# Kernel tuning notes

Measured on AMD Instinct MI355X. Metric: run time of the kernel, lower is better.

The kernel has to match this reference:

```python
import jax, jax.numpy as jnp
import numpy as np

DIM = 768
H = 12
HEAD = DIM // H
SCALE = HEAD ** -0.5
NMM, NV, NA = 8, 4, 4


def _cross_attn(x1, x2, qw, kvw, pw, pb):
    # x1: [B,N1,C] queries, x2: [B,N2,C] keys/values. Weights stored [in,out].
    B, N1, C = x1.shape
    N2 = x2.shape[1]
    q = (x1 @ qw).reshape(B, N1, H, HEAD).transpose(0, 2, 1, 3)        # [B,H,N1,d]
    kv = (x2 @ kvw).reshape(B, N2, 2, H, HEAD)
    k = kv[:, :, 0].transpose(0, 2, 1, 3)                               # [B,H,N2,d]
    v = kv[:, :, 1].transpose(0, 2, 1, 3)
    attn = jax.nn.softmax(jnp.einsum('bhnd,bhmd->bhnm', q, k) * SCALE, axis=-1)
    o = jnp.einsum('bhnm,bhmd->bhnd', attn, v).transpose(0, 2, 1, 3).reshape(B, N1, C)
    return o @ pw + pb, attn


def setup_inputs() -> dict:
    key = jax.random.key(0)
    ks = jax.random.split(key, 16)
    s = 0.02
    inp = {
        'xmm': jax.random.normal(ks[0], (64, 16, DIM), jnp.float32),
        'xv': jax.random.normal(ks[1], (64, 784, DIM), jnp.float32),
        'xa': jax.random.normal(ks[2], (64, 512, DIM), jnp.float32),
        # visual cross-attn params (weights stored [in,out] = torch W.T)
        'qv_w': s * jax.random.normal(ks[3], (DIM, DIM), jnp.float32),
        'kvv_w': s * jax.random.normal(ks[4], (DIM, 2 * DIM), jnp.float32),
        'projv_w': s * jax.random.normal(ks[5], (DIM, DIM), jnp.float32),
        'projv_b': jnp.zeros((DIM,), jnp.float32),
        # audio cross-attn params
        'qa_w': s * jax.random.normal(ks[6], (DIM, DIM), jnp.float32),
        'kva_w': s * jax.random.normal(ks[7], (DIM, 2 * DIM), jnp.float32),
        'proja_w': s * jax.random.normal(ks[8], (DIM, DIM), jnp.float32),
        'proja_b': jnp.zeros((DIM,), jnp.float32),
        # factorized fusion attention params (dim_ratio=1.0 -> inner dim = DIM)
        'fq_w': s * jax.random.normal(ks[9], (DIM, DIM), jnp.float32),
        'fk_w': s * jax.random.normal(ks[10], (2 * DIM, DIM), jnp.float32),
        'fv_w': s * jax.random.normal(ks[11], (2 * DIM, DIM), jnp.float32),
        'fproj_w': s * jax.random.normal(ks[12], (DIM, DIM), jnp.float32),
        'fproj_b': jnp.zeros((DIM,), jnp.float32),
    }
    return inp


def reference(xmm, xv, xa, qv_w, kvv_w, projv_w, projv_b,
              qa_w, kva_w, proja_w, proja_b,
              fq_w, fk_w, fv_w, fproj_w, fproj_b):
    B = xmm.shape[0]
    xmm2 = xmm[:, :NMM]
    xmm_v, _ = _cross_attn(xmm[:, NMM:NMM + NV], xv, qv_w, kvv_w, projv_w, projv_b)
    xmm_a, _ = _cross_attn(xmm[:, NMM + NV:], xa, qa_w, kva_w, proja_w, proja_b)
    # outer-product token fusion: [B, NV*NA, 2*DIM]
    xva = jnp.concatenate([
        jnp.broadcast_to(xmm_v[:, :, None, :], (B, NV, NA, DIM)),
        jnp.broadcast_to(xmm_a[:, None, :, :], (B, NV, NA, DIM)),
    ], axis=-1).reshape(B, NV * NA, 2 * DIM)
    q = (xmm2 @ fq_w).reshape(B, NMM, H, -1).transpose(0, 2, 1, 3)
    k = (xva @ fk_w).reshape(B, NV * NA, H, -1).transpose(0, 2, 1, 3)
    v = (xva @ fv_w).reshape(B, NV * NA, H, -1).transpose(0, 2, 1, 3)
    attn = jax.nn.softmax(jnp.einsum('bhnd,bhmd->bhnm', q, k) * SCALE, axis=-1)
    o = jnp.einsum('bhnm,bhmd->bhnd', attn, v).transpose(0, 2, 1, 3).reshape(B, NMM, DIM)
    o = o @ fproj_w + fproj_b
    xmm_out = jnp.concatenate([o, xmm_v, xmm_a], axis=1)  # [B,16,DIM]
    return xmm_out, attn
```

## Files before the change

kernel.cpp:

```cpp
#include <hip/hip_runtime.h>
#include <stdint.h>

typedef unsigned short u16;
typedef unsigned int u32;
typedef __attribute__((ext_vector_type(8))) short short8;
typedef __attribute__((ext_vector_type(4))) float floatx4;


__device__ __forceinline__ u16 f2bf_rne(float f) {
  u32 u = __float_as_uint(f);
  return (u16)((u + 0x7fffu + ((u >> 16) & 1u)) >> 16);
}
__device__ __forceinline__ u32 pack_rne_u(u32 a, u32 b) {
  a += 0x7fffu + ((a >> 16) & 1u);
  b += 0x7fffu + ((b >> 16) & 1u);
  return __builtin_amdgcn_perm(b, a, 0x07060302u);
}
__device__ __forceinline__ void gld_lds16(const void* g, void* l) {
  __builtin_amdgcn_global_load_lds(
      (__attribute__((address_space(1))) void*)(uintptr_t)g,
      (__attribute__((address_space(3))) void*)l, 16, 0, 0);
}

__device__ __forceinline__ void sg_body(
    float (*sAt)[20], float (*sW)[64],
    const float* __restrict__ A, int a_pitch, int a_rb, int a_off,
    const float* __restrict__ W, const float* __restrict__ bias,
    float* __restrict__ Cout, int c_pitch, int c_rb, int c_off,
    int rt, int n0)
{
  const int t = threadIdx.x;
  const int g = t >> 6;
  const int c = t & 63;

  float acc[4] = {0.f, 0.f, 0.f, 0.f};

  for (int ks = 0; ks < 12; ++ks) {
    {
      int r = t >> 4;
      int c4 = (t & 15) * 4;
      int lr = rt * 16 + r;
      int grow = (lr / a_rb) * a_pitch + a_off + (lr % a_rb);
      float4 v = *(const float4*)(A + (size_t)grow * 768 + ks * 64 + c4);
      sAt[c4 + 0][r] = v.x;
      sAt[c4 + 1][r] = v.y;
      sAt[c4 + 2][r] = v.z;
      sAt[c4 + 3][r] = v.w;
    }
#pragma unroll
    for (int u = 0; u < 4; ++u) {
      int unit = t + u * 256;
      int r = unit >> 4;
      int c4 = (unit & 15) * 4;
      *(float4*)&sW[r][c4] = *(const float4*)(W + (size_t)(ks * 64 + r) * 768 + n0 + c4);
    }
    __syncthreads();
#pragma unroll 8
    for (int k = 0; k < 64; ++k) {
      float4 a4 = *(const float4*)&sAt[k][g * 4];
      float w = sW[k][c];
      acc[0] += a4.x * w;
      acc[1] += a4.y * w;
      acc[2] += a4.z * w;
      acc[3] += a4.w * w;
    }
    __syncthreads();
  }

  float bs = bias ? bias[n0 + c] : 0.f;
#pragma unroll
  for (int rr = 0; rr < 4; ++rr) {
    int lr = rt * 16 + g * 4 + rr;
    int grow = (lr / c_rb) * c_pitch + c_off + (lr % c_rb);
    Cout[(size_t)grow * 768 + n0 + c] = acc[rr] + bs;
  }
}

__global__ __launch_bounds__(256) void qproj(
    const float* __restrict__ xmm,
    const float* __restrict__ qv_w, const float* __restrict__ qa_w,
    const float* __restrict__ fq_w,
    float* __restrict__ q_v, float* __restrict__ q_a, float* __restrict__ q_f)
{
  __shared__ float sAt[64][20];
  __shared__ float sW[64][64];
  int rt = blockIdx.x;
  int n0 = blockIdx.y * 64;
  if (rt < 16)
    sg_body(sAt, sW, xmm, 16, 4, 8, qv_w, nullptr, q_v, 4, 4, 0, rt, n0);
  else if (rt < 32)
    sg_body(sAt, sW, xmm, 16, 4, 12, qa_w, nullptr, q_a, 4, 4, 0, rt - 16, n0);
  else
    sg_body(sAt, sW, xmm, 16, 8, 0, fq_w, nullptr, q_f, 8, 8, 0, rt - 32, n0);
}

__global__ __launch_bounds__(256) void proj2(
    const float* __restrict__ o_v, const float* __restrict__ o_a,
    const float* __restrict__ projv_w, const float* __restrict__ projv_b,
    const float* __restrict__ proja_w, const float* __restrict__ proja_b,
    float* __restrict__ out0)
{
  __shared__ float sAt[64][20];
  __shared__ float sW[64][64];
  int z = blockIdx.z;
  sg_body(sAt, sW, z ? o_a : o_v, 4, 4, 0,
          z ? proja_w : projv_w, z ? proja_b : projv_b,
          out0, 16, 4, z ? 12 : 8, blockIdx.x, blockIdx.y * 64);
}

__global__ __launch_bounds__(256) void fkv(
    const float* __restrict__ out0,
    const float* __restrict__ fk_w, const float* __restrict__ fv_w,
    float* __restrict__ kbase)
{
  __shared__ float sAt[64][20];
  __shared__ float sW[64][64];
  int z = blockIdx.z;
  const float* W = (z < 2) ? (fk_w + (size_t)(z & 1) * 768 * 768)
                           : (fv_w + (size_t)(z & 1) * 768 * 768);
  int a_off = (z & 1) ? 12 : 8;
  sg_body(sAt, sW, out0, 16, 4, a_off, W, nullptr,
          kbase + (size_t)z * 256 * 768, 4, 4, 0, blockIdx.x, blockIdx.y * 64);
}

__global__ __launch_bounds__(256) void fproj(
    const float* __restrict__ o_f,
    const float* __restrict__ fproj_w, const float* __restrict__ fproj_b,
    float* __restrict__ out0)
{
  __shared__ float sAt[64][20];
  __shared__ float sW[64][64];
  sg_body(sAt, sW, o_f, 8, 8, 0, fproj_w, fproj_b, out0, 16, 8, 0,
          blockIdx.x, blockIdx.y * 64);
}

__global__ __launch_bounds__(256) void qtilde(
    const float* __restrict__ q_v, const float* __restrict__ q_a,
    const float* __restrict__ kvv_w, const float* __restrict__ kva_w,
    u16* __restrict__ Qt_v, u16* __restrict__ Qt_a)
{
  __shared__ float sAt[64][20];
  __shared__ float sW[64][65];

  const int rt = blockIdx.x;
  const int nt = blockIdx.y;
  const int path = blockIdx.z / 12;
  const int h = blockIdx.z % 12;
  const float* q = path ? q_a : q_v;
  const float* kvw = path ? kva_w : kvv_w;
  u16* Qt = path ? Qt_a : Qt_v;

  const int t = threadIdx.x;
  const int g = t >> 6;
  const int c = t & 63;
  const int n0 = nt * 64;

  {
    int r = t >> 4;
    int c4 = (t & 15) * 4;
    float4 v = *(const float4*)(q + (size_t)(rt * 16 + r) * 768 + h * 64 + c4);
    sAt[c4 + 0][r] = v.x;
    sAt[c4 + 1][r] = v.y;
    sAt[c4 + 2][r] = v.z;
    sAt[c4 + 3][r] = v.w;
  }
#pragma unroll
  for (int u = 0; u < 4; ++u) {
    int unit = t + u * 256;
    int d = unit >> 4;
    int c4 = (unit & 15) * 4;
    float4 v = *(const float4*)(kvw + (size_t)(n0 + d) * 1536 + h * 64 + c4);
    sW[d][c4 + 0] = v.x;
    sW[d][c4 + 1] = v.y;
    sW[d][c4 + 2] = v.z;
    sW[d][c4 + 3] = v.w;
  }
  __syncthreads();

  float acc[4] = {0.f, 0.f, 0.f, 0.f};
#pragma unroll 16
  for (int e = 0; e < 64; ++e) {
    float4 a4 = *(const float4*)&sAt[e][g * 4];
    float w = sW[c][e];
    acc[0] += a4.x * w;
    acc[1] += a4.y * w;
    acc[2] += a4.z * w;
    acc[3] += a4.w * w;
  }
#pragma unroll
  for (int rr = 0; rr < 4; ++rr) {
    int rl = rt * 16 + g * 4 + rr;
    Qt[((size_t)(rl >> 2) * 48 + h * 4 + (rl & 3)) * 768 + n0 + c] = f2bf_rne(acc[rr]);
  }
}

__global__ __launch_bounds__(256) void attn_logits(
    const u16* __restrict__ Qt_v, const u16* __restrict__ Qt_a,
    const float* __restrict__ Xv, const float* __restrict__ Xa,
    float* __restrict__ Sv, float* __restrict__ Sa)
{
  const int z = blockIdx.z;
  const int jt = blockIdx.x;
  if (z == 1 && jt >= 4) return;
  const u16* Qt = z ? Qt_a : Qt_v;
  const float* X = z ? Xa : Xv;
  float* S = z ? Sa : Sv;
  const int N2 = z ? 512 : 784;

  __shared__ __align__(16) u16 sQ[48 * 64];
  __shared__ __align__(16) u16 sX[128 * 64];

  const int t = threadIdx.x;
  const int lane = t & 63;
  const int wave = t >> 6;
  const int b = blockIdx.y;
  const int j0 = jt * 128;
  const int jmax = (N2 - j0 < 128) ? (N2 - j0) : 128;
  const u16* Qb = Qt + (size_t)b * 48 * 768;
  const float* Xb = X + (size_t)b * N2 * 768;

  floatx4 acc[3][2];
#pragma unroll
  for (int i = 0; i < 3; ++i)
#pragma unroll
    for (int j = 0; j < 2; ++j) acc[i][j] = (floatx4){0.f, 0.f, 0.f, 0.f};

  for (int ks = 0; ks < 12; ++ks) {
    {
      int chunk = wave;
      int row = chunk * 8 + (lane >> 3);
      gld_lds16(Qb + (size_t)row * 768 + ks * 64 + (lane & 7) * 8,
                (char*)sQ + chunk * 1024);
      chunk = wave + 4;
      if (chunk < 6) {
        row = chunk * 8 + (lane >> 3);
        gld_lds16(Qb + (size_t)row * 768 + ks * 64 + (lane & 7) * 8,
                  (char*)sQ + chunk * 1024);
      }
    }
#pragma unroll
    for (int u = 0; u < 4; ++u) {
      int unit = t + u * 256;
      int r = unit >> 3;
      int c8 = unit & 7;
      uint4 pk = (uint4){0u, 0u, 0u, 0u};
      if (r < jmax) {
        const uint4* src = (const uint4*)(Xb + (size_t)(j0 + r) * 768 + ks * 64 + c8 * 8);
        uint4 x0 = src[0];
        uint4 x1 = src[1];
        pk.x = pack_rne_u(x0.x, x0.y);
        pk.y = pack_rne_u(x0.z, x0.w);
        pk.z = pack_rne_u(x1.x, x1.y);
        pk.w = pack_rne_u(x1.z, x1.w);
      }
      *(uint4*)(sX + r * 64 + ((c8 * 8) ^ ((r & 7) * 8))) = pk;
    }
    __syncthreads();
#pragma unroll
    for (int kk = 0; kk < 2; ++kk) {
      short8 af[3], bfr[2];
#pragma unroll
      for (int i = 0; i < 3; ++i)
        af[i] = *(const short8*)(sQ + (i * 16 + (lane & 15)) * 64 + kk * 32 + (lane >> 4) * 8);
#pragma unroll
      for (int jj = 0; jj < 2; ++jj) {
        int jr = wave * 32 + jj * 16 + (lane & 15);
        int kb = kk * 32 + (lane >> 4) * 8;
        bfr[jj] = *(const short8*)(sX + jr * 64 + (kb ^ ((jr & 7) * 8)));
      }
#pragma unroll
      for (int i = 0; i < 3; ++i)
#pragma unroll
        for (int jj = 0; jj < 2; ++jj)
          acc[i][jj] = __builtin_amdgcn_mfma_f32_16x16x32_bf16(af[i], bfr[jj], acc[i][jj], 0, 0, 0);
    }
    __syncthreads();
  }

  const int quad = lane >> 4;
  const int lc = lane & 15;
#pragma unroll
  for (int i = 0; i < 3; ++i)
#pragma unroll
    for (int jj = 0; jj < 2; ++jj) {
      int col = j0 + wave * 32 + jj * 16 + lc;
      if (col < N2) {
        int row0 = i * 16 + quad * 4;
#pragma unroll
        for (int r = 0; r < 4; ++r)
          S[((size_t)b * 48 + row0 + r) * N2 + col] = acc[i][jj][r] * 0.125f;
      }
    }
}

__global__ __launch_bounds__(256) void softmax_p(
    const float* __restrict__ Sv, const float* __restrict__ Sa,
    u16* __restrict__ Pv, u16* __restrict__ Pa)
{
  const int z = blockIdx.z;
  const float* S = z ? Sa : Sv;
  u16* P = z ? Pa : Pv;
  const int N2 = z ? 512 : 784;
  const int N2p = z ? 512 : 832;

  const int hh = blockIdx.x;
  const int b = blockIdx.y;
  const int t = threadIdx.x;
  const int lane = t & 63;
  const int wave = t >> 6;
  const int row = hh * 4 + wave;
  const float* Srow = S + ((size_t)b * 48 + row) * N2;
  u16* Prow = P + ((size_t)b * 48 + row) * N2p;

  float m = -1e30f;
  for (int j = lane; j < N2; j += 64) m = fmaxf(m, Srow[j]);
#pragma unroll
  for (int off = 32; off > 0; off >>= 1) m = fmaxf(m, __shfl_xor(m, off));

  float e[13];
  float l = 0.f;
  int cnt = 0;
  for (int j = lane; j < N2; j += 64) {
    float p = __expf(Srow[j] - m);
    e[cnt++] = p;
    l += p;
  }
#pragma unroll
  for (int off = 32; off > 0; off >>= 1) l += __shfl_xor(l, off);
  float inv = 1.0f / l;

  cnt = 0;
  for (int j = lane; j < N2; j += 64) Prow[j] = f2bf_rne(e[cnt++] * inv);
  for (int j = N2 + lane; j < N2p; j += 64) Prow[j] = 0;
}

__global__ __launch_bounds__(256) void attn_px(
    const u16* __restrict__ Pv, const u16* __restrict__ Pa,
    const float* __restrict__ Xv, const float* __restrict__ Xa,
    float* __restrict__ Ov, float* __restrict__ Oa)
{
  const int z = blockIdx.z;
  const u16* P = z ? Pa : Pv;
  const float* X = z ? Xa : Xv;
  float* O = z ? Oa : Ov;
  const int N2 = z ? 512 : 784;
  const int N2p = z ? 512 : 832;

  __shared__ __align__(16) u16 sP[48 * 64];
  __shared__ __align__(16) u16 sXT[128 * 72];

  const int t = threadIdx.x;
  const int lane = t & 63;
  const int wave = t >> 6;
  const int nt = blockIdx.x;
  const int b = blockIdx.y;
  const int n0 = nt * 128;
  const u16* Pb = P + (size_t)b * 48 * N2p;
  const float* Xb = X + (size_t)b * N2 * 768;
  const int Ks = N2p >> 6;

  floatx4 acc[3][2];
#pragma unroll
  for (int i = 0; i < 3; ++i)
#pragma unroll
    for (int j = 0; j < 2; ++j) acc[i][j] = (floatx4){0.f, 0.f, 0.f, 0.f};

  for (int ks = 0; ks < Ks; ++ks) {
    {
      int chunk = wave;
      int row = chunk * 8 + (lane >> 3);
      gld_lds16(Pb + (size_t)row * N2p + ks * 64 + (lane & 7) * 8,
                (char*)sP + chunk * 1024);
      chunk = wave + 4;
      if (chunk < 6) {
        row = chunk * 8 + (lane >> 3);
        gld_lds16(Pb + (size_t)row * N2p + ks * 64 + (lane & 7) * 8,
                  (char*)sP + chunk * 1024);
      }
    }
#pragma unroll
    for (int u = 0; u < 4; ++u) {
      int unit = t + u * 256;
      int jp = unit >> 5;
      int nq = unit & 31;
      int j = ks * 64 + jp * 2;
      int n4 = nq * 4;
      uint4 xa = (uint4){0u, 0u, 0u, 0u};
      uint4 xb = (uint4){0u, 0u, 0u, 0u};
      if (j < N2)     xa = *(const uint4*)(Xb + (size_t)j * 768 + n0 + n4);
      if (j + 1 < N2) xb = *(const uint4*)(Xb + (size_t)(j + 1) * 768 + n0 + n4);
      u32 w0 = pack_rne_u(xa.x, xb.x);
      u32 w1 = pack_rne_u(xa.y, xb.y);
      u32 w2 = pack_rne_u(xa.z, xb.z);
      u32 w3 = pack_rne_u(xa.w, xb.w);
      int jl = jp * 2;
#pragma unroll
      for (int m = 0; m < 4; ++m) {
        int n = n4 + m;
        int sw = (((n >> 2) & 7) ^ ((n & 3) << 1)) * 8;
        u32 wv = (m == 0) ? w0 : (m == 1) ? w1 : (m == 2) ? w2 : w3;
        *(u32*)&sXT[n * 72 + (jl ^ sw)] = wv;
      }
    }
    __syncthreads();
#pragma unroll
    for (int kk = 0; kk < 2; ++kk) {
      short8 af[3];
#pragma unroll
      for (int i = 0; i < 3; ++i)
        af[i] = *(const short8*)(sP + (i * 16 + (lane & 15)) * 64 + kk * 32 + (lane >> 4) * 8);
#pragma unroll
      for (int jj = 0; jj < 2; ++jj) {
        int n = wave * 32 + jj * 16 + (lane & 15);
        int sw = (((n >> 2) & 7) ^ ((n & 3) << 1)) * 8;
        int kb = kk * 32 + (lane >> 4) * 8;
        short8 bfr = *(const short8*)&sXT[n * 72 + (kb ^ sw)];
#pragma unroll
        for (int i = 0; i < 3; ++i)
          acc[i][jj] = __builtin_amdgcn_mfma_f32_16x16x32_bf16(af[i], bfr, acc[i][jj], 0, 0, 0);
      }
    }
    __syncthreads();
  }

  const int quad = lane >> 4;
  const int lc = lane & 15;
#pragma unroll
  for (int i = 0; i < 3; ++i)
#pragma unroll
    for (int jj = 0; jj < 2; ++jj) {
      int col = n0 + wave * 32 + jj * 16 + lc;
      int row0 = i * 16 + quad * 4;
#pragma unroll
      for (int r = 0; r < 4; ++r)
        O[((size_t)b * 48 + row0 + r) * 768 + col] = acc[i][jj][r];
    }
}

__global__ __launch_bounds__(256) void omix(
    const float* __restrict__ O_v, const float* __restrict__ O_a,
    const float* __restrict__ kvv_w, const float* __restrict__ kva_w,
    float* __restrict__ o_v, float* __restrict__ o_a)
{
  __shared__ float sAt[64][20];
  __shared__ float sW[64][64];

  const int z = blockIdx.z;
  const float* Ob = z ? O_a : O_v;
  const float* kvw = z ? kva_w : kvv_w;
  float* oo = z ? o_a : o_v;

  const int rt = blockIdx.x;
  const int h = blockIdx.y;
  const int t = threadIdx.x;
  const int g = t >> 6;
  const int c = t & 63;

  float acc[4] = {0.f, 0.f, 0.f, 0.f};

  for (int ks = 0; ks < 12; ++ks) {
    {
      int r = t >> 4;
      int c4 = (t & 15) * 4;
      int rl = rt * 16 + r;
      int arow = (rl >> 2) * 48 + h * 4 + (rl & 3);
      float4 v = *(const float4*)(Ob + (size_t)arow * 768 + ks * 64 + c4);
      sAt[c4 + 0][r] = v.x;
      sAt[c4 + 1][r] = v.y;
      sAt[c4 + 2][r] = v.z;
      sAt[c4 + 3][r] = v.w;
    }
#pragma unroll
    for (int u = 0; u < 4; ++u) {
      int unit = t + u * 256;
      int k = unit >> 4;
      int c4 = (unit & 15) * 4;
      *(float4*)&sW[k][c4] = *(const float4*)(kvw + (size_t)(ks * 64 + k) * 1536 + 768 + h * 64 + c4);
    }
    __syncthreads();
#pragma unroll 8
    for (int k = 0; k < 64; ++k) {
      float4 a4 = *(const float4*)&sAt[k][g * 4];
      float w = sW[k][c];
      acc[0] += a4.x * w;
      acc[1] += a4.y * w;
      acc[2] += a4.z * w;
      acc[3] += a4.w * w;
    }
    __syncthreads();
  }

#pragma unroll
  for (int rr = 0; rr < 4; ++rr) {
    int rl = rt * 16 + g * 4 + rr;
    oo[(size_t)rl * 768 + h * 64 + c] = acc[rr];
  }
}

__global__ __launch_bounds__(256) void fusion_attn(
    const float* __restrict__ Qf,
    const float* __restrict__ K1, const float* __restrict__ K2,
    const float* __restrict__ V1, const float* __restrict__ V2,
    float* __restrict__ Of,
    float* __restrict__ AttnOut)
{
  const int h = blockIdx.x;
  const int b = blockIdx.y;
  const int t = threadIdx.x;
  const int lane = t & 63;
  const int wave = t >> 6;

  __shared__ float sQ[8][64];
  __shared__ float sK1[4][64], sK2[4][64], sV1[4][64], sV2[4][64];
  __shared__ float sP[8][16];

  for (int idx = t; idx < 512; idx += 256)
    sQ[idx >> 6][idx & 63] = Qf[((size_t)(b * 8 + (idx >> 6))) * 768 + h * 64 + (idx & 63)];
  {
    size_t base = ((size_t)(b * 4 + wave)) * 768 + h * 64 + lane;
    sK1[wave][lane] = K1[base];
    sK2[wave][lane] = K2[base];
    sV1[wave][lane] = V1[base];
    sV2[wave][lane] = V2[base];
  }
  __syncthreads();

  if (t < 128) {
    int qi = t >> 4, m = t & 15, iv = m >> 2, ja = m & 3;
    float s = 0.f;
#pragma unroll
    for (int d = 0; d < 64; ++d) s += sQ[qi][d] * (sK1[iv][d] + sK2[ja][d]);
    s *= 0.125f;
    float mx = s;
#pragma unroll
    for (int off = 8; off > 0; off >>= 1) mx = fmaxf(mx, __shfl_xor(mx, off, 16));
    float p = __expf(s - mx);
    float l = p;
#pragma unroll
    for (int off = 8; off > 0; off >>= 1) l += __shfl_xor(l, off, 16);
    p = p / l;
    sP[qi][m] = p;
    AttnOut[(((size_t)b * 12 + h) * 8 + qi) * 16 + m] = p;
  }
  __syncthreads();

  for (int idx = t; idx < 512; idx += 256) {
    int qi = idx >> 6, d = idx & 63;
    float o = 0.f;
#pragma unroll
    for (int m = 0; m < 16; ++m) o += sP[qi][m] * (sV1[m >> 2][d] + sV2[m & 3][d]);
    Of[((size_t)(b * 8 + qi)) * 768 + h * 64 + d] = o;
  }
}

extern "C" void kernel_launch(void* const* d_in, const int* in_sizes, int n_in,
                              void* d_out, int out_size, void* d_ws, size_t ws_size,
                              hipStream_t stream)
{
  const float* xmm     = (const float*)d_in[0];
  const float* xv      = (const float*)d_in[1];
  const float* xa      = (const float*)d_in[2];
  const float* qv_w    = (const float*)d_in[3];
  const float* kvv_w   = (const float*)d_in[4];
  const float* projv_w = (const float*)d_in[5];
  const float* projv_b = (const float*)d_in[6];
  const float* qa_w    = (const float*)d_in[7];
  const float* kva_w   = (const float*)d_in[8];
  const float* proja_w = (const float*)d_in[9];
  const float* proja_b = (const float*)d_in[10];
  const float* fq_w    = (const float*)d_in[11];
  const float* fk_w    = (const float*)d_in[12];
  const float* fv_w    = (const float*)d_in[13];
  const float* fproj_w = (const float*)d_in[14];
  const float* fproj_b = (const float*)d_in[15];

  float* out0 = (float*)d_out;
  float* out1 = out0 + (size_t)64 * 16 * 768;

  char* ws = (char*)d_ws;
  size_t off = 0;
  float* q_v  = (float*)(ws + off); off += (size_t)256 * 768 * 4;
  float* q_a  = (float*)(ws + off); off += (size_t)256 * 768 * 4;
  float* q_f  = (float*)(ws + off); off += (size_t)512 * 768 * 4;
  u16*   Qt_v = (u16*)(ws + off);   off += (size_t)64 * 48 * 768 * 2;
  u16*   Qt_a = (u16*)(ws + off);   off += (size_t)64 * 48 * 768 * 2;
  float* S_v  = (float*)(ws + off); off += (size_t)64 * 48 * 784 * 4;
  float* S_a  = (float*)(ws + off); off += (size_t)64 * 48 * 512 * 4;
  u16*   P_v  = (u16*)(ws + off);   off += (size_t)64 * 48 * 832 * 2;
  u16*   P_a  = (u16*)(ws + off);   off += (size_t)64 * 48 * 512 * 2;
  float* O_v  = (float*)(ws + off); off += (size_t)64 * 48 * 768 * 4;
  float* O_a  = (float*)(ws + off); off += (size_t)64 * 48 * 768 * 4;
  float* o_v  = (float*)(ws + off); off += (size_t)256 * 768 * 4;
  float* o_a  = (float*)(ws + off); off += (size_t)256 * 768 * 4;
  float* kbase = (float*)(ws + off); off += (size_t)4 * 256 * 768 * 4;
  float* o_f  = (float*)(ws + off); off += (size_t)512 * 768 * 4;

  float* k1 = kbase;
  float* k2 = kbase + (size_t)256 * 768;
  float* v1 = kbase + (size_t)2 * 256 * 768;
  float* v2 = kbase + (size_t)3 * 256 * 768;

  qproj<<<dim3(64, 12), 256, 0, stream>>>(xmm, qv_w, qa_w, fq_w, q_v, q_a, q_f);
  qtilde<<<dim3(16, 12, 24), 256, 0, stream>>>(q_v, q_a, kvv_w, kva_w, Qt_v, Qt_a);
  attn_logits<<<dim3(7, 64, 2), 256, 0, stream>>>(Qt_v, Qt_a, xv, xa, S_v, S_a);
  softmax_p<<<dim3(12, 64, 2), 256, 0, stream>>>(S_v, S_a, P_v, P_a);
  attn_px<<<dim3(6, 64, 2), 256, 0, stream>>>(P_v, P_a, xv, xa, O_v, O_a);
  omix<<<dim3(16, 12, 2), 256, 0, stream>>>(O_v, O_a, kvv_w, kva_w, o_v, o_a);
  proj2<<<dim3(16, 12, 2), 256, 0, stream>>>(o_v, o_a, projv_w, projv_b, proja_w, proja_b, out0);
  fkv<<<dim3(16, 12, 4), 256, 0, stream>>>(out0, fk_w, fv_w, kbase);
  fusion_attn<<<dim3(12, 64), 256, 0, stream>>>(q_f, k1, k2, v1, v2, o_f, out1);
  fproj<<<dim3(32, 12), 256, 0, stream>>>(o_f, fproj_w, fproj_b, out0);
}
```

Measured before the change: 590.8 us.

## Double-buffer LDS and prefetch X/Q into registers in attention GEMM kernels

```diff
diff --git a/kernel.cpp b/kernel.cpp
--- a/kernel.cpp
+++ b/kernel.cpp
@@ -16,10 +16,11 @@
   b += 0x7fffu + ((b >> 16) & 1u);
   return __builtin_amdgcn_perm(b, a, 0x07060302u);
 }
-__device__ __forceinline__ void gld_lds16(const void* g, void* l) {
-  __builtin_amdgcn_global_load_lds(
-      (__attribute__((address_space(1))) void*)(uintptr_t)g,
-      (__attribute__((address_space(3))) void*)l, 16, 0, 0);
+
+__device__ __forceinline__ void block_sync_lds() {
+  asm volatile("s_waitcnt lgkmcnt(0)" ::: "memory");
+  __builtin_amdgcn_s_barrier();
+  asm volatile("" ::: "memory");
 }
 
 __device__ __forceinline__ void sg_body(
@@ -207,8 +208,7 @@
   float* S = z ? Sa : Sv;
   const int N2 = z ? 512 : 784;
 
-  __shared__ __align__(16) u16 sQ[48 * 64];
-  __shared__ __align__(16) u16 sX[128 * 64];
+  __shared__ __align__(16) u16 sX[2][128 * 64];
 
   const int t = threadIdx.x;
   const int lane = t & 63;
@@ -219,63 +219,96 @@
   const u16* Qb = Qt + (size_t)b * 48 * 768;
   const float* Xb = X + (size_t)b * N2 * 768;
 
+  const int xr_r = t >> 3;
+  const int xc = (t & 7) * 8;
+  const int qrow0 = lane & 15;
+  const int qcb = (lane >> 4) * 8;
+
   floatx4 acc[3][2];
 #pragma unroll
   for (int i = 0; i < 3; ++i)
 #pragma unroll
     for (int j = 0; j < 2; ++j) acc[i][j] = (floatx4){0.f, 0.f, 0.f, 0.f};
 
-  for (int ks = 0; ks < 12; ++ks) {
-    {
-      int chunk = wave;
-      int row = chunk * 8 + (lane >> 3);
-      gld_lds16(Qb + (size_t)row * 768 + ks * 64 + (lane & 7) * 8,
-                (char*)sQ + chunk * 1024);
-      chunk = wave + 4;
-      if (chunk < 6) {
-        row = chunk * 8 + (lane >> 3);
-        gld_lds16(Qb + (size_t)row * 768 + ks * 64 + (lane & 7) * 8,
-                  (char*)sQ + chunk * 1024);
-      }
-    }
-#pragma unroll
-    for (int u = 0; u < 4; ++u) {
-      int unit = t + u * 256;
-      int r = unit >> 3;
-      int c8 = unit & 7;
-      uint4 pk = (uint4){0u, 0u, 0u, 0u};
-      if (r < jmax) {
-        const uint4* src = (const uint4*)(Xb + (size_t)(j0 + r) * 768 + ks * 64 + c8 * 8);
-        uint4 x0 = src[0];
-        uint4 x1 = src[1];
-        pk.x = pack_rne_u(x0.x, x0.y);
-        pk.y = pack_rne_u(x0.z, x0.w);
-        pk.z = pack_rne_u(x1.x, x1.y);
-        pk.w = pack_rne_u(x1.z, x1.w);
-      }
-      *(uint4*)(sX + r * 64 + ((c8 * 8) ^ ((r & 7) * 8))) = pk;
-    }
-    __syncthreads();
-#pragma unroll
-    for (int kk = 0; kk < 2; ++kk) {
-      short8 af[3], bfr[2];
-#pragma unroll
-      for (int i = 0; i < 3; ++i)
-        af[i] = *(const short8*)(sQ + (i * 16 + (lane & 15)) * 64 + kk * 32 + (lane >> 4) * 8);
-#pragma unroll
-      for (int jj = 0; jj < 2; ++jj) {
-        int jr = wave * 32 + jj * 16 + (lane & 15);
-        int kb = kk * 32 + (lane >> 4) * 8;
-        bfr[jj] = *(const short8*)(sX + jr * 64 + (kb ^ ((jr & 7) * 8)));
-      }
-#pragma unroll
-      for (int i = 0; i < 3; ++i)
-#pragma unroll
-        for (int jj = 0; jj < 2; ++jj)
-          acc[i][jj] = __builtin_amdgcn_mfma_f32_16x16x32_bf16(af[i], bfr[jj], acc[i][jj], 0, 0, 0);
-    }
-    __syncthreads();
-  }
+  uint4 xA[4][2], xB[4][2];
+  short8 qr[3][2];
+
+#define AL_LOADX(dst, ks_)                                                     \
+  do {                                                                         \
+    _Pragma("unroll") for (int u = 0; u < 4; ++u) {                            \
+      int r_ = xr_r + u * 32;                                                  \
+      uint4 a0_ = {0u, 0u, 0u, 0u}, a1_ = {0u, 0u, 0u, 0u};                    \
+      if (r_ < jmax) {                                                         \
+        const uint4* s_ =                                                      \
+            (const uint4*)(Xb + (size_t)(j0 + r_) * 768 + (ks_) * 64 + xc);    \
+        a0_ = s_[0];                                                           \
+        a1_ = s_[1];                                                           \
+      }                                                                        \
+      dst[u][0] = a0_;                                                         \
+      dst[u][1] = a1_;                                                         \
+    }                                                                          \
+  } while (0)
+
+#define AL_LOADQ(ks_)                                                          \
+  do {                                                                         \
+    _Pragma("unroll") for (int i = 0; i < 3; ++i)                              \
+      _Pragma("unroll") for (int kk = 0; kk < 2; ++kk)                         \
+        qr[i][kk] = *(const short8*)(Qb + (size_t)(i * 16 + qrow0) * 768 +     \
+                                     (ks_) * 64 + kk * 32 + qcb);              \
+  } while (0)
+
+#define AL_WRITEX(src, bufp)                                                   \
+  do {                                                                         \
+    _Pragma("unroll") for (int u = 0; u < 4; ++u) {                            \
+      int r_ = xr_r + u * 32;                                                  \
+      uint4 pk_;                                                               \
+      pk_.x = pack_rne_u(src[u][0].x, src[u][0].y);                            \
+      pk_.y = pack_rne_u(src[u][0].z, src[u][0].w);                            \
+      pk_.z = pack_rne_u(src[u][1].x, src[u][1].y);                            \
+      pk_.w = pack_rne_u(src[u][1].z, src[u][1].w);                            \
+      *(uint4*)((bufp) + r_ * 64 + (xc ^ ((r_ & 7) * 8))) = pk_;               \
+    }                                                                          \
+  } while (0)
+
+#define AL_COMPUTE(bufp)                                                       \
+  do {                                                                         \
+    _Pragma("unroll") for (int kk = 0; kk < 2; ++kk) {                         \
+      short8 bfr_[2];                                                          \
+      _Pragma("unroll") for (int jj = 0; jj < 2; ++jj) {                       \
+        int jr_ = wave * 32 + jj * 16 + qrow0;                                 \
+        int kb_ = kk * 32 + qcb;                                               \
+        bfr_[jj] =                                                             \
+            *(const short8*)((bufp) + jr_ * 64 + (kb_ ^ ((jr_ & 7) * 8)));     \
+      }                                                                        \
+      _Pragma("unroll") for (int i = 0; i < 3; ++i)                            \
+        _Pragma("unroll") for (int jj = 0; jj < 2; ++jj)                       \
+          acc[i][jj] = __builtin_amdgcn_mfma_f32_16x16x32_bf16(                \
+              qr[i][kk], bfr_[jj], acc[i][jj], 0, 0, 0);                       \
+    }                                                                          \
+  } while (0)
+
+  u16* sX0 = &sX[0][0];
+  u16* sX1 = &sX[1][0];
+
+  AL_LOADX(xA, 0);
+  AL_LOADQ(0);
+#pragma unroll
+  for (int ks = 0; ks < 12; ks += 2) {
+    AL_LOADX(xB, ks + 1);
+    AL_WRITEX(xA, sX0);
+    block_sync_lds();
+    AL_COMPUTE(sX0);
+    AL_LOADQ(ks + 1);
+    if (ks + 2 < 12) AL_LOADX(xA, ks + 2);
+    AL_WRITEX(xB, sX1);
+    block_sync_lds();
+    AL_COMPUTE(sX1);
+    if (ks + 2 < 12) AL_LOADQ(ks + 2);
+  }
+#undef AL_LOADX
+#undef AL_LOADQ
+#undef AL_WRITEX
+#undef AL_COMPUTE
 
   const int quad = lane >> 4;
   const int lc = lane & 15;
@@ -346,8 +379,7 @@
   const int N2 = z ? 512 : 784;
   const int N2p = z ? 512 : 832;
 
-  __shared__ __align__(16) u16 sP[48 * 64];
-  __shared__ __align__(16) u16 sXT[128 * 72];
+  __shared__ __align__(16) u16 sXT[2][128 * 72];
 
   const int t = threadIdx.x;
   const int lane = t & 63;
@@ -359,69 +391,102 @@
   const float* Xb = X + (size_t)b * N2 * 768;
   const int Ks = N2p >> 6;
 
+  const int jp0 = t >> 5;
+  const int nq4 = (t & 31) * 4;
+  const int qrow0 = lane & 15;
+  const int qcb = (lane >> 4) * 8;
+
   floatx4 acc[3][2];
 #pragma unroll
   for (int i = 0; i < 3; ++i)
 #pragma unroll
     for (int j = 0; j < 2; ++j) acc[i][j] = (floatx4){0.f, 0.f, 0.f, 0.f};
 
-  for (int ks = 0; ks < Ks; ++ks) {
-    {
-      int chunk = wave;
-      int row = chunk * 8 + (lane >> 3);
-      gld_lds16(Pb + (size_t)row * N2p + ks * 64 + (lane & 7) * 8,
-                (char*)sP + chunk * 1024);
-      chunk = wave + 4;
-      if (chunk < 6) {
-        row = chunk * 8 + (lane >> 3);
-        gld_lds16(Pb + (size_t)row * N2p + ks * 64 + (lane & 7) * 8,
-                  (char*)sP + chunk * 1024);
-      }
-    }
-#pragma unroll
-    for (int u = 0; u < 4; ++u) {
-      int unit = t + u * 256;
-      int jp = unit >> 5;
-      int nq = unit & 31;
-      int j = ks * 64 + jp * 2;
-      int n4 = nq * 4;
-      uint4 xa = (uint4){0u, 0u, 0u, 0u};
-      uint4 xb = (uint4){0u, 0u, 0u, 0u};
-      if (j < N2)     xa = *(const uint4*)(Xb + (size_t)j * 768 + n0 + n4);
-      if (j + 1 < N2) xb = *(const uint4*)(Xb + (size_t)(j + 1) * 768 + n0 + n4);
-      u32 w0 = pack_rne_u(xa.x, xb.x);
-      u32 w1 = pack_rne_u(xa.y, xb.y);
-      u32 w2 = pack_rne_u(xa.z, xb.z);
-      u32 w3 = pack_rne_u(xa.w, xb.w);
-      int jl = jp * 2;
-#pragma unroll
-      for (int m = 0; m < 4; ++m) {
-        int n = n4 + m;
-        int sw = (((n >> 2) & 7) ^ ((n & 3) << 1)) * 8;
-        u32 wv = (m == 0) ? w0 : (m == 1) ? w1 : (m == 2) ? w2 : w3;
-        *(u32*)&sXT[n * 72 + (jl ^ sw)] = wv;
-      }
-    }
-    __syncthreads();
-#pragma unroll
-    for (int kk = 0; kk < 2; ++kk) {
-      short8 af[3];
-#pragma unroll
-      for (int i = 0; i < 3; ++i)
-        af[i] = *(const short8*)(sP + (i * 16 + (lane & 15)) * 64 + kk * 32 + (lane >> 4) * 8);
-#pragma unroll
-      for (int jj = 0; jj < 2; ++jj) {
-        int n = wave * 32 + jj * 16 + (lane & 15);
-        int sw = (((n >> 2) & 7) ^ ((n & 3) << 1)) * 8;
-        int kb = kk * 32 + (lane >> 4) * 8;
-        short8 bfr = *(const short8*)&sXT[n * 72 + (kb ^ sw)];
-#pragma unroll
-        for (int i = 0; i < 3; ++i)
-          acc[i][jj] = __builtin_amdgcn_mfma_f32_16x16x32_bf16(af[i], bfr, acc[i][jj], 0, 0, 0);
-      }
-    }
-    __syncthreads();
-  }
+  uint4 xA[4][2], xB[4][2];
+  short8 qr[3][2];
+
+#define PX_LOADX(dst, ks_)                                                     \
+  do {                                                                         \
+    _Pragma("unroll") for (int u = 0; u < 4; ++u) {                            \
+      int j_ = (ks_) * 64 + (jp0 + u * 8) * 2;                                 \
+      uint4 a0_ = {0u, 0u, 0u, 0u}, a1_ = {0u, 0u, 0u, 0u};                    \
+      if (j_ < N2)                                                             \
+        a0_ = *(const uint4*)(Xb + (size_t)j_ * 768 + n0 + nq4);               \
+      if (j_ + 1 < N2)                                                         \
+        a1_ = *(const uint4*)(Xb + (size_t)(j_ + 1) * 768 + n0 + nq4);         \
+      dst[u][0] = a0_;                                                         \
+      dst[u][1] = a1_;                                                         \
+    }                                                                          \
+  } while (0)
+
+#define PX_LOADP(ks_)                                                          \
+  do {                                                                         \
+    _Pragma("unroll") for (int i = 0; i < 3; ++i)                              \
+      _Pragma("unroll") for (int kk = 0; kk < 2; ++kk)                         \
+        qr[i][kk] = *(const short8*)(Pb + (size_t)(i * 16 + qrow0) * N2p +     \
+                                     (ks_) * 64 + kk * 32 + qcb);              \
+  } while (0)
+
+#define PX_WRITEX(src, bufp)                                                   \
+  do {                                                                         \
+    _Pragma("unroll") for (int u = 0; u < 4; ++u) {                            \
+      int jl_ = (jp0 + u * 8) * 2;                                             \
+      u32 w0_ = pack_rne_u(src[u][0].x, src[u][1].x);                          \
+      u32 w1_ = pack_rne_u(src[u][0].y, src[u][1].y);                          \
+      u32 w2_ = pack_rne_u(src[u][0].z, src[u][1].z);                          \
+      u32 w3_ = pack_rne_u(src[u][0].w, src[u][1].w);                          \
+      _Pragma("unroll") for (int m_ = 0; m_ < 4; ++m_) {                       \
+        int n_ = nq4 + m_;                                                     \
+        int sw_ = (((n_ >> 2) & 7) ^ ((n_ & 3) << 1)) * 8;                     \
+        u32 wv_ = (m_ == 0) ? w0_ : (m_ == 1) ? w1_ : (m_ == 2) ? w2_ : w3_;   \
+        *(u32*)((bufp) + n_ * 72 + (jl_ ^ sw_)) = wv_;                         \
+      }                                                                        \
+    }                                                                          \
+  } while (0)
+
+#define PX_COMPUTE(bufp)                                                       \
+  do {                                                                         \
+    _Pragma("unroll") for (int kk = 0; kk < 2; ++kk) {                         \
+      _Pragma("unroll") for (int jj = 0; jj < 2; ++jj) {                       \
+        int n_ = wave * 32 + jj * 16 + qrow0;                                  \
+        int sw_ = (((n_ >> 2) & 7) ^ ((n_ & 3) << 1)) * 8;                     \
+        int kb_ = kk * 32 + qcb;                                               \
+        short8 bfr_ = *(const short8*)((bufp) + n_ * 72 + (kb_ ^ sw_));        \
+        _Pragma("unroll") for (int i = 0; i < 3; ++i)                          \
+          acc[i][jj] = __builtin_amdgcn_mfma_f32_16x16x32_bf16(                \
+              qr[i][kk], bfr_, acc[i][jj], 0, 0, 0);                           \
+      }                                                                        \
+    }                                                                          \
+  } while (0)
+
+  u16* sT0 = &sXT[0][0];
+  u16* sT1 = &sXT[1][0];
+
+  PX_LOADX(xA, 0);
+  PX_LOADP(0);
+  int ks = 0;
+  for (;;) {
+    int more0 = (ks + 1 < Ks);
+    if (more0) PX_LOADX(xB, ks + 1);
+    PX_WRITEX(xA, sT0);
+    block_sync_lds();
+    PX_COMPUTE(sT0);
+    if (!more0) break;
+    PX_LOADP(ks + 1);
+    ++ks;
+    int more1 = (ks + 1 < Ks);
+    if (more1) PX_LOADX(xA, ks + 1);
+    PX_WRITEX(xB, sT1);
+    block_sync_lds();
+    PX_COMPUTE(sT1);
+    if (!more1) break;
+    PX_LOADP(ks + 1);
+    ++ks;
+  }
+#undef PX_LOADX
+#undef PX_LOADP
+#undef PX_WRITEX
+#undef PX_COMPUTE
 
   const int quad = lane >> 4;
   const int lc = lane & 15;
```

After: 589.1 us. About the same (-0.3%).
